# Optimization experiments

Hardware: AMD Instinct MI355X
Metric: run time of the kernel (lower is better)

## Reference

```python
import jax, jax.numpy as jnp
import numpy as np

S, B, E, H = 2048, 4, 1024, 16
HD = E // H
EPS = 1e-8


def _bit_linear(x, W, b):
    """BitNetLinear (eval): ternary weight quant + abs-mean activation scaling."""
    w_scale = jnp.maximum(jnp.mean(jnp.abs(W)), EPS)
    wn = W / w_scale
    qw = jnp.sign(wn) * (jnp.abs(wn) > 0.5).astype(x.dtype)  # {-1,0,1}
    a_scale = jnp.maximum(jnp.mean(jnp.abs(x)), EPS)
    out = (x / a_scale) @ (qw * w_scale).T + b
    return out * a_scale


def setup_inputs() -> dict:
    key = jax.random.key(0)
    ks = jax.random.split(key, 9)
    # xavier-uniform-ish init for [E,E] weights
    lim = float(np.sqrt(6.0 / (E + E)))
    def w(k):
        return jax.random.uniform(k, (E, E), jnp.float32, -lim, lim)
    return {
        "query": jax.random.normal(ks[0], (S, B, E), jnp.float32),
        "Wq": w(ks[1]), "bq": jnp.zeros((E,), jnp.float32),
        "Wk": w(ks[2]), "bk": jnp.zeros((E,), jnp.float32),
        "Wv": w(ks[3]), "bv": jnp.zeros((E,), jnp.float32),
        "Wo": w(ks[4]), "bo": jnp.zeros((E,), jnp.float32),
    }


def reference(query, Wq, bq, Wk, bk, Wv, bv, Wo, bo):
    q = _bit_linear(query, Wq, bq)  # [S,B,E]
    k = _bit_linear(query, Wk, bk)
    v = _bit_linear(query, Wv, bv)
    # [S,B,E] -> [B*H, S, HD]
    def split_heads(t):
        return t.reshape(S, B * H, HD).transpose(1, 0, 2)
    q, k, v = split_heads(q), split_heads(k), split_heads(v)
    scaling = HD ** -0.5
    scores = jnp.einsum("nqd,nkd->nqk", q, k) * scaling  # [B*H,S,S]
    probs = jax.nn.softmax(scores, axis=-1)
    attn = jnp.einsum("nqk,nkd->nqd", probs, v)  # [B*H,S,HD]
    attn = attn.transpose(1, 0, 2).reshape(S, B, E)
    out = _bit_linear(attn, Wo, bo)  # [S,B,E]
    # need_weights=True, average_attn_weights=True -> mean over heads
    attn_weights = probs.reshape(B, H, S, S).mean(axis=1)  # [B,S,S]
    return out, attn_weights
```

## Files before the change

### kernel.cpp

```cpp
#include <hip/hip_runtime.h>


typedef __bf16 bf16_t;
typedef __bf16 bf16x8 __attribute__((ext_vector_type(8)));
typedef float  f32x4  __attribute__((ext_vector_type(4)));

#define MFMA16(Af, Bf, Cv) __builtin_amdgcn_mfma_f32_16x16x32_bf16((Af), (Bf), (Cv), 0, 0, 0)
#define EXP2(x) __builtin_amdgcn_exp2f(x)

constexpr float LOG2E   = 1.4426950408889634f;
constexpr float SHIFT2  = 14.426950408889634f;
constexpr float QSCALE  = 0.125f * LOG2E;

__device__ __forceinline__ void gload16(const void* g, void* l) {
  __builtin_amdgcn_global_load_lds(
      (const __attribute__((address_space(1))) void*)g,
      (__attribute__((address_space(3))) void*)l, 16, 0, 0);
}

__device__ __forceinline__ void stage8k(const bf16_t* __restrict__ g0, int gstride,
                                        char* ldsb, int tid, int w) {
  const int rr = tid >> 3;
  const int cs = ((tid & 7) * 8) ^ ((rr & 7) * 8);
  gload16(g0 + (size_t)rr * gstride + cs, ldsb + w * 1024);
  gload16(g0 + (size_t)(rr + 32) * gstride + cs, ldsb + 4096 + w * 1024);
}

__device__ __forceinline__ void stage8k512(const bf16_t* __restrict__ g0, int gstride,
                                           char* ldsb, int tid) {
  const int rr = tid >> 3;
  const int cs = ((tid & 7) * 8) ^ ((rr & 7) * 8);
  gload16(g0 + (size_t)rr * gstride + cs, ldsb + (tid >> 6) * 1024);
}

__device__ __forceinline__ bf16x8 lds_frag(const char* ldsb, int row, int bytecol) {
  return *(const bf16x8*)(ldsb + row * 128 + (bytecol ^ ((row & 7) << 4)));
}

constexpr int S_ = 2048, B_ = 4, E_ = 1024, H_ = 16, HD_ = 64;
constexpr int M_ = S_ * B_;
constexpr int NH_ = B_ * H_;

constexpr size_t OFF_SCALES = 0;
constexpr size_t OFF_PART   = 256;
constexpr size_t OFF_XB     = 8192;
constexpr size_t SZ_X       = (size_t)M_ * E_ * 2;
constexpr size_t OFF_TQKV   = OFF_XB + SZ_X;
constexpr size_t OFF_TO     = OFF_TQKV + (size_t)3072 * 1024 * 2;
constexpr size_t OFF_QH     = OFF_TO + (size_t)1024 * 1024 * 2;
constexpr size_t SZ_HD      = (size_t)NH_ * S_ * HD_ * 2;
constexpr size_t OFF_KH     = OFF_QH + SZ_HD;
constexpr size_t OFF_VT     = OFF_KH + SZ_HD;
constexpr size_t OFF_STL    = OFF_VT + SZ_HD;
constexpr size_t OFF_ATTN   = OFF_STL + (size_t)NH_ * S_ * 4;

__global__ void k_prep_all(const float4* __restrict__ W0, const float4* __restrict__ W1,
                           const float4* __restrict__ W2, const float4* __restrict__ W3,
                           const float4* __restrict__ X, ushort4* __restrict__ Xb,
                           float* __restrict__ part) {
  const int bid = blockIdx.x;
  float s = 0.f;
  if (bid < 1024) {
    const int seg = bid >> 8, blk = bid & 255;
    const float4* src = (seg == 0) ? W0 : (seg == 1) ? W1 : (seg == 2) ? W2 : W3;
    for (int i = blk * 256 + threadIdx.x; i < 262144; i += 65536) {
      float4 x = src[i];
      s += fabsf(x.x) + fabsf(x.y) + fabsf(x.z) + fabsf(x.w);
    }
  } else {
    for (int i = (bid - 1024) * 256 + threadIdx.x; i < 2097152; i += 65536) {
      float4 v = X[i];
      s += fabsf(v.x) + fabsf(v.y) + fabsf(v.z) + fabsf(v.w);
      ushort4 h;
      h.x = __builtin_bit_cast(unsigned short, (__bf16)v.x);
      h.y = __builtin_bit_cast(unsigned short, (__bf16)v.y);
      h.z = __builtin_bit_cast(unsigned short, (__bf16)v.z);
      h.w = __builtin_bit_cast(unsigned short, (__bf16)v.w);
      Xb[i] = h;
    }
  }
  __shared__ float red[256];
  red[threadIdx.x] = s; __syncthreads();
  for (int st = 128; st > 0; st >>= 1) {
    if (threadIdx.x < st) red[threadIdx.x] += red[threadIdx.x + st];
    __syncthreads();
  }
  if (threadIdx.x == 0) part[bid] = red[0];
}

__global__ void k_finalize(const float* __restrict__ part, float* __restrict__ scales,
                           int r0, int r1) {
  __shared__ float red[256];
  int t = threadIdx.x;
  for (int r = r0; r < r1; ++r) {
    red[t] = part[r * 256 + t];
    __syncthreads();
    for (int st = 128; st > 0; st >>= 1) {
      if (t < st) red[t] += red[t + st];
      __syncthreads();
    }
    if (t == 0) {
      float cnt = (r < 4) ? 1048576.0f : 8388608.0f;
      scales[r] = fmaxf(red[0] / cnt, 1e-8f);
    }
    __syncthreads();
  }
}

__device__ __forceinline__ unsigned short tern_u(float w, float wsc) {
  float wn = w / wsc;
  if (!(fabsf(wn) > 0.5f)) return 0;
  return (wn > 0.f) ? (unsigned short)0x3F80 : (unsigned short)0xBF80;
}

__global__ void k_quantize4(const float4* __restrict__ W0, const float4* __restrict__ W1,
                            const float4* __restrict__ W2, const float4* __restrict__ W3,
                            const float* __restrict__ scales,
                            ushort4* __restrict__ T0, ushort4* __restrict__ T1,
                            ushort4* __restrict__ T2, ushort4* __restrict__ T3) {
  const int seg = blockIdx.x >> 10;
  const int i = (blockIdx.x & 1023) * 256 + threadIdx.x;
  const float4* W = (seg == 0) ? W0 : (seg == 1) ? W1 : (seg == 2) ? W2 : W3;
  ushort4* T = (seg == 0) ? T0 : (seg == 1) ? T1 : (seg == 2) ? T2 : T3;
  float wsc = scales[seg];
  float4 w = W[i];
  ushort4 o;
  o.x = tern_u(w.x, wsc); o.y = tern_u(w.y, wsc);
  o.z = tern_u(w.z, wsc); o.w = tern_u(w.w, wsc);
  T[i] = o;
}

__global__ __launch_bounds__(256) void k_gemm_qkv(
    const bf16_t* __restrict__ Xb, const bf16_t* __restrict__ T,
    const float* __restrict__ scales,
    const float* __restrict__ bq, const float* __restrict__ bk, const float* __restrict__ bv,
    bf16_t* __restrict__ Qh, bf16_t* __restrict__ Kh, bf16_t* __restrict__ Vt) {
  __shared__ char lds[32768];
  const int tid = threadIdx.x, w = tid >> 6, lane = tid & 63;
  const int g = lane >> 4, cc = lane & 15;
  const int l = blockIdx.x;
  const int xcd = l & 7, r = l >> 3;
  const int nIdx = r % 24, mloc = r / 24;
  const int bm = (xcd * 8 + mloc) * 128, bn = nIdx * 128;
  const int wm = (w >> 1) * 64, wn = (w & 1) * 64;
  const int subA = wm >> 6, subB = wn >> 6;
  f32x4 acc[4][4] = {};
  for (int kt = 0; kt < 16; ++kt) {
    const int k0 = kt * 64;
    const bf16_t* xa = &Xb[(size_t)bm * 1024 + k0];
    const bf16_t* tb = &T[(size_t)bn * 1024 + k0];
    stage8k(xa, 1024, lds, tid, w);
    stage8k(xa + 64 * 1024, 1024, lds + 8192, tid, w);
    stage8k(tb, 1024, lds + 16384, tid, w);
    stage8k(tb + 64 * 1024, 1024, lds + 24576, tid, w);
    __syncthreads();
    const char* As = lds + subA * 8192;
    const char* Bs = lds + 16384 + subB * 8192;
    #pragma unroll
    for (int ks = 0; ks < 2; ++ks) {
      bf16x8 af[4], bfr[4];
      #pragma unroll
      for (int i = 0; i < 4; ++i)
        af[i] = lds_frag(As, (wm & 63) + i * 16 + cc, ks * 64 + g * 16);
      #pragma unroll
      for (int j = 0; j < 4; ++j)
        bfr[j] = lds_frag(Bs, (wn & 63) + j * 16 + cc, ks * 64 + g * 16);
      __builtin_amdgcn_s_setprio(1);
      #pragma unroll
      for (int i = 0; i < 4; ++i)
        #pragma unroll
        for (int j = 0; j < 4; ++j)
          acc[i][j] = MFMA16(af[i], bfr[j], acc[i][j]);
      __builtin_amdgcn_s_setprio(0);
    }
    __syncthreads();
  }
  const int seg = bn >> 10;
  const float wsc = scales[seg];
  const float asx = scales[4];
  const float* bias = (seg == 0) ? bq : (seg == 1) ? bk : bv;
  #pragma unroll
  for (int i = 0; i < 4; ++i)
    #pragma unroll
    for (int j = 0; j < 4; ++j)
      #pragma unroll
      for (int r2 = 0; r2 < 4; ++r2) {
        int m = bm + wm + i * 16 + g * 4 + r2;
        int n = bn + wn + j * 16 + cc;
        int e = n & 1023;
        float v = acc[i][j][r2] * wsc + bias[e] * asx;
        int s = m >> 2, b = m & 3, h = e >> 6, d = e & 63;
        if (seg == 0) {
          Qh[((b * 16 + h) * 2048 + s) * 64 + d] = (bf16_t)(v * QSCALE);
        } else if (seg == 1) {
          Kh[((b * 16 + h) * 2048 + s) * 64 + d] = (bf16_t)v;
        } else {
          Vt[((b * 16 + h) * 64 + d) * 2048 + s] = (bf16_t)v;
        }
      }
}

__global__ __launch_bounds__(512) void k_flash(
    const bf16_t* __restrict__ Qh, const bf16_t* __restrict__ Kh,
    const bf16_t* __restrict__ Vt,
    bf16_t* __restrict__ attnb, float* __restrict__ stl) {
  __shared__ char lds[81920];
  char* Ps = lds + 49152;
  const int tid = threadIdx.x, w = tid >> 6, lane = tid & 63;
  const int g = lane >> 4, cc = lane & 15;
  const int l = blockIdx.x;
  const int head = (l & 7) * 8 + ((l >> 3) & 7);
  const int q0 = (l >> 6) * 256;
  const int qbaseA = (head * 2048 + q0 + w * 32 + cc) * 64 + g * 8;
  const int qbaseB = qbaseA + 16 * 64;
  const bf16x8 qa0 = *(const bf16x8*)&Qh[qbaseA];
  const bf16x8 qa1 = *(const bf16x8*)&Qh[qbaseA + 32];
  const bf16x8 qb0 = *(const bf16x8*)&Qh[qbaseB];
  const bf16x8 qb1 = *(const bf16x8*)&Qh[qbaseB + 32];
  const bf16_t* Kb = Kh + (size_t)head * 2048 * 64;
  const bf16_t* Vb = Vt + (size_t)head * 64 * 2048;
  const bf16_t one_b = (bf16_t)1.0f;
  const bf16x8 ones = {one_b, one_b, one_b, one_b, one_b, one_b, one_b, one_b};
  const f32x4 minit = {-SHIFT2, -SHIFT2, -SHIFT2, -SHIFT2};
  f32x4 accOA[4] = {}, accOB[4] = {};
  f32x4 accLA = {}, accLB = {};
  stage8k512(Kb, 64, lds, tid);
  stage8k512(Vb, 2048, lds + 24576, tid);
  stage8k512(Kb + 64 * 64, 64, lds + 8192, tid);
  stage8k512(Vb + 64, 2048, lds + 24576 + 8192, tid);
  int cur = 0;
  for (int t = 0; t < 32; ++t) {
    if (t < 31) asm volatile("s_waitcnt vmcnt(2)" ::: "memory");
    else        asm volatile("s_waitcnt vmcnt(0)" ::: "memory");
    __builtin_amdgcn_s_barrier();
    if (t + 2 < 32) {
      int nb = cur + 2; if (nb >= 3) nb -= 3;
      stage8k512(Kb + (t + 2) * 64 * 64, 64, lds + nb * 8192, tid);
      stage8k512(Vb + (t + 2) * 64, 2048, lds + 24576 + nb * 8192, tid);
    }
    const char* KhL = lds + cur * 8192;
    const char* VtL = lds + 24576 + cur * 8192;
    f32x4 sA[4], sB[4];
    #pragma unroll
    for (int nf = 0; nf < 4; ++nf) { sA[nf] = minit; sB[nf] = minit; }
    __builtin_amdgcn_s_setprio(1);
    #pragma unroll
    for (int nf = 0; nf < 4; ++nf) {
      const int row = nf * 16 + cc;
      bf16x8 kh0 = lds_frag(KhL, row, g * 16);
      bf16x8 kh1 = lds_frag(KhL, row, 64 + g * 16);
      sA[nf] = MFMA16(qa0, kh0, sA[nf]);
      sA[nf] = MFMA16(qa1, kh1, sA[nf]);
      sB[nf] = MFMA16(qb0, kh0, sB[nf]);
      sB[nf] = MFMA16(qb1, kh1, sB[nf]);
    }
    __builtin_amdgcn_s_setprio(0);
    #pragma unroll
    for (int nf = 0; nf < 4; ++nf)
      #pragma unroll
      for (int r = 0; r < 4; ++r) {
        float pA = EXP2(sA[nf][r]);
        float pB = EXP2(sB[nf][r]);
        int rowA = w * 32 + g * 4 + r;
        int rowB = rowA + 16;
        int colb = (nf * 16 + cc) * 2;
        *(bf16_t*)(Ps + ((rowA * 128 + colb) ^ ((rowA & 7) << 4))) = (bf16_t)pA;
        *(bf16_t*)(Ps + ((rowB * 128 + colb) ^ ((rowB & 7) << 4))) = (bf16_t)pB;
      }
    const int prA = w * 32 + cc, prB = prA + 16;
    const int pbA = (prA * 128 + g * 16) ^ ((prA & 7) << 4);
    const int pbB = (prB * 128 + g * 16) ^ ((prB & 7) << 4);
    const bf16x8 paA0 = *(const bf16x8*)(Ps + pbA);
    const bf16x8 paA1 = *(const bf16x8*)(Ps + (pbA ^ 64));
    const bf16x8 paB0 = *(const bf16x8*)(Ps + pbB);
    const bf16x8 paB1 = *(const bf16x8*)(Ps + (pbB ^ 64));
    __builtin_amdgcn_s_setprio(1);
    accLA = MFMA16(paA0, ones, accLA);
    accLA = MFMA16(paA1, ones, accLA);
    accLB = MFMA16(paB0, ones, accLB);
    accLB = MFMA16(paB1, ones, accLB);
    #pragma unroll
    for (int df = 0; df < 4; ++df) {
      const int row = df * 16 + cc;
      bf16x8 v0 = lds_frag(VtL, row, g * 16);
      bf16x8 v1 = lds_frag(VtL, row, 64 + g * 16);
      accOA[df] = MFMA16(paA0, v0, accOA[df]);
      accOA[df] = MFMA16(paA1, v1, accOA[df]);
      accOB[df] = MFMA16(paB0, v0, accOB[df]);
      accOB[df] = MFMA16(paB1, v1, accOB[df]);
    }
    __builtin_amdgcn_s_setprio(0);
    cur = cur + 1; if (cur >= 3) cur = 0;
  }
  const int b = head >> 4, h = head & 15;
  #pragma unroll
  for (int df = 0; df < 4; ++df)
    #pragma unroll
    for (int r = 0; r < 4; ++r) {
      int qA = q0 + w * 32 + g * 4 + r;
      int e = h * 64 + df * 16 + cc;
      attnb[(qA * 4 + b) * 1024 + e] = (bf16_t)(accOA[df][r] / accLA[r]);
      attnb[((qA + 16) * 4 + b) * 1024 + e] = (bf16_t)(accOB[df][r] / accLB[r]);
    }
  if (cc == 0) {
    #pragma unroll
    for (int r = 0; r < 4; ++r) {
      int qA = q0 + w * 32 + g * 4 + r;
      stl[head * 2048 + qA] = accLA[r];
      stl[head * 2048 + qA + 16] = accLB[r];
    }
  }
}

__global__ __launch_bounds__(256) void k_pm(
    const bf16_t* __restrict__ Qh, const bf16_t* __restrict__ Kh,
    const float* __restrict__ stl, float* __restrict__ aw) {
  __shared__ char kbuf[2 * 16384];
  __shared__ float sc_[2048];
  const int tid = threadIdx.x, w = tid >> 6, lane = tid & 63;
  const int g = lane >> 4, cc = lane & 15;
  const int l = blockIdx.x;
  const int q0 = (l & 15) * 128, b = (l >> 4) & 3, z = l >> 6;
  const int kbeg = z * 128;
  for (int i = tid; i < 2048; i += 256) {
    int h = i >> 7, q = i & 127;
    sc_[i] = -log2f(stl[(b * 16 + h) * 2048 + q0 + q]) - SHIFT2;
  }
  __syncthreads();
  stage8k(Kh + ((size_t)(b * 16 + 0) * 2048 + kbeg) * 64, 64, kbuf, tid, w);
  stage8k(Kh + ((size_t)(b * 16 + 1) * 2048 + kbeg) * 64, 64, kbuf + 8192, tid, w);
  int cur = 0;
  float pmA[4][4], pmB[4][4];
  for (int it = 0; it < 16; ++it) {
    const int kt = it >> 3, hp = it & 7;
    const int ktl = kbeg + kt * 64;
    asm volatile("s_waitcnt vmcnt(0)" ::: "memory");
    __builtin_amdgcn_s_barrier();
    if (it + 1 < 16) {
      const int nx = it + 1;
      const int ktn = kbeg + (nx >> 3) * 64, hpn = nx & 7;
      char* nb = kbuf + (cur ^ 1) * 16384;
      stage8k(Kh + ((size_t)(b * 16 + 2 * hpn) * 2048 + ktn) * 64, 64, nb, tid, w);
      stage8k(Kh + ((size_t)(b * 16 + 2 * hpn + 1) * 2048 + ktn) * 64, 64, nb + 8192, tid, w);
    }
    if (hp == 0) {
      #pragma unroll
      for (int nf = 0; nf < 4; ++nf)
        #pragma unroll
        for (int r = 0; r < 4; ++r) { pmA[nf][r] = 0.f; pmB[nf][r] = 0.f; }
    }
    #pragma unroll
    for (int hi = 0; hi < 2; ++hi) {
      const int h = 2 * hp + hi;
      const int head = b * 16 + h;
      const int qbaseA = (head * 2048 + q0 + w * 32 + cc) * 64 + g * 8;
      const int qbaseB = qbaseA + 16 * 64;
      bf16x8 qa0 = *(const bf16x8*)&Qh[qbaseA];
      bf16x8 qa1 = *(const bf16x8*)&Qh[qbaseA + 32];
      bf16x8 qb0 = *(const bf16x8*)&Qh[qbaseB];
      bf16x8 qb1 = *(const bf16x8*)&Qh[qbaseB + 32];
      f32x4 ciA, ciB;
      #pragma unroll
      for (int r = 0; r < 4; ++r) {
        int qloc = w * 32 + g * 4 + r;
        ciA[r] = sc_[h * 128 + qloc];
        ciB[r] = sc_[h * 128 + qloc + 16];
      }
      const char* KhL = kbuf + cur * 16384 + hi * 8192;
      f32x4 sA[4], sB[4];
      #pragma unroll
      for (int nf = 0; nf < 4; ++nf) { sA[nf] = ciA; sB[nf] = ciB; }
      __builtin_amdgcn_s_setprio(1);
      #pragma unroll
      for (int nf = 0; nf < 4; ++nf) {
        const int row = nf * 16 + cc;
        bf16x8 kh0 = lds_frag(KhL, row, g * 16);
        bf16x8 kh1 = lds_frag(KhL, row, 64 + g * 16);
        sA[nf] = MFMA16(qa0, kh0, sA[nf]);
        sA[nf] = MFMA16(qa1, kh1, sA[nf]);
        sB[nf] = MFMA16(qb0, kh0, sB[nf]);
        sB[nf] = MFMA16(qb1, kh1, sB[nf]);
      }
      __builtin_amdgcn_s_setprio(0);
      #pragma unroll
      for (int nf = 0; nf < 4; ++nf)
        #pragma unroll
        for (int r = 0; r < 4; ++r) {
          pmA[nf][r] += EXP2(sA[nf][r]);
          pmB[nf][r] += EXP2(sB[nf][r]);
        }
    }
    if (hp == 7) {
      #pragma unroll
      for (int nf = 0; nf < 4; ++nf)
        #pragma unroll
        for (int r = 0; r < 4; ++r) {
          int qA = q0 + w * 32 + g * 4 + r;
          int k = ktl + nf * 16 + cc;
          aw[((long)(b * 2048 + qA)) * 2048 + k] = pmA[nf][r] * 0.0625f;
          aw[((long)(b * 2048 + qA + 16)) * 2048 + k] = pmB[nf][r] * 0.0625f;
        }
    }
    cur ^= 1;
  }
}

__global__ __launch_bounds__(256) void k_gemm_out(
    const bf16_t* __restrict__ A, const bf16_t* __restrict__ T,
    const float* __restrict__ scales, const float* __restrict__ bo,
    float* __restrict__ out) {
  __shared__ char lds[32768];
  const int tid = threadIdx.x, w = tid >> 6, lane = tid & 63;
  const int g = lane >> 4, cc = lane & 15;
  const int l = blockIdx.x;
  const int xcd = l & 7, r = l >> 3;
  const int nIdx = r & 7, mloc = r >> 3;
  const int bm = (xcd * 8 + mloc) * 128, bn = nIdx * 128;
  const int wm = (w >> 1) * 64, wn = (w & 1) * 64;
  const int subA = wm >> 6, subB = wn >> 6;
  f32x4 acc[4][4] = {};
  for (int kt = 0; kt < 16; ++kt) {
    const int k0 = kt * 64;
    const bf16_t* aa = &A[(size_t)bm * 1024 + k0];
    const bf16_t* tb = &T[(size_t)bn * 1024 + k0];
    stage8k(aa, 1024, lds, tid, w);
    stage8k(aa + 64 * 1024, 1024, lds + 8192, tid, w);
    stage8k(tb, 1024, lds + 16384, tid, w);
    stage8k(tb + 64 * 1024, 1024, lds + 24576, tid, w);
    __syncthreads();
    const char* As = lds + subA * 8192;
    const char* Bs = lds + 16384 + subB * 8192;
    #pragma unroll
    for (int ks = 0; ks < 2; ++ks) {
      bf16x8 af[4], bfr[4];
      #pragma unroll
      for (int i = 0; i < 4; ++i)
        af[i] = lds_frag(As, (wm & 63) + i * 16 + cc, ks * 64 + g * 16);
      #pragma unroll
      for (int j = 0; j < 4; ++j)
        bfr[j] = lds_frag(Bs, (wn & 63) + j * 16 + cc, ks * 64 + g * 16);
      __builtin_amdgcn_s_setprio(1);
      #pragma unroll
      for (int i = 0; i < 4; ++i)
        #pragma unroll
        for (int j = 0; j < 4; ++j)
          acc[i][j] = MFMA16(af[i], bfr[j], acc[i][j]);
      __builtin_amdgcn_s_setprio(0);
    }
    __syncthreads();
  }
  const float wsc = scales[3];
  #pragma unroll
  for (int i = 0; i < 4; ++i)
    #pragma unroll
    for (int j = 0; j < 4; ++j)
      #pragma unroll
      for (int r2 = 0; r2 < 4; ++r2) {
        int m = bm + wm + i * 16 + g * 4 + r2;
        int n = bn + wn + j * 16 + cc;
        out[m * 1024 + n] = acc[i][j][r2] * wsc + bo[n];
      }
}

extern "C" void kernel_launch(void* const* d_in, const int* in_sizes, int n_in,
                              void* d_out, int out_size, void* d_ws, size_t ws_size,
                              hipStream_t stream) {
  (void)in_sizes; (void)n_in; (void)out_size; (void)ws_size;
  const float* query = (const float*)d_in[0];
  const float* Wq = (const float*)d_in[1];
  const float* bq = (const float*)d_in[2];
  const float* Wk = (const float*)d_in[3];
  const float* bk = (const float*)d_in[4];
  const float* Wv = (const float*)d_in[5];
  const float* bv = (const float*)d_in[6];
  const float* Wo = (const float*)d_in[7];
  const float* bo = (const float*)d_in[8];

  char* ws = (char*)d_ws;
  float*  scales = (float*)(ws + OFF_SCALES);
  float*  part   = (float*)(ws + OFF_PART);
  bf16_t* Xb     = (bf16_t*)(ws + OFF_XB);
  bf16_t* Tqkv   = (bf16_t*)(ws + OFF_TQKV);
  bf16_t* To     = (bf16_t*)(ws + OFF_TO);
  bf16_t* Qh     = (bf16_t*)(ws + OFF_QH);
  bf16_t* Kh     = (bf16_t*)(ws + OFF_KH);
  bf16_t* Vt     = (bf16_t*)(ws + OFF_VT);
  float*  Stl    = (float*)(ws + OFF_STL);
  bf16_t* Attn   = (bf16_t*)(ws + OFF_ATTN);

  float* out0 = (float*)d_out;
  float* aw   = out0 + (size_t)M_ * E_;

  k_prep_all<<<1280, 256, 0, stream>>>((const float4*)Wq, (const float4*)Wk,
                                       (const float4*)Wv, (const float4*)Wo,
                                       (const float4*)query, (ushort4*)Xb, part);
  k_finalize<<<1, 256, 0, stream>>>(part, scales, 0, 5);
  k_quantize4<<<4096, 256, 0, stream>>>((const float4*)Wq, (const float4*)Wk,
                                        (const float4*)Wv, (const float4*)Wo, scales,
                                        (ushort4*)Tqkv, (ushort4*)(Tqkv + 1048576),
                                        (ushort4*)(Tqkv + 2097152), (ushort4*)To);

  k_gemm_qkv<<<1536, 256, 0, stream>>>(Xb, Tqkv, scales, bq, bk, bv, Qh, Kh, Vt);
  k_flash<<<512, 512, 0, stream>>>(Qh, Kh, Vt, Attn, Stl);
  k_pm<<<1024, 256, 0, stream>>>(Qh, Kh, Stl, aw);
  k_gemm_out<<<512, 256, 0, stream>>>(Attn, To, scales, bo, out0);
}
```

Before: 296.5 us.

## Fold scale finalize into consumers and merge prob-mean and output GEMM launches

Removes the single-block k_finalize launch: each consumer block (quantize, QKV GEMM epilogue, output GEMM epilogue) now reduces the 256 partial sums itself to get its scale. k_pm and k_gemm_out become one k_tail launch, with blocks split by index between the two jobs so they can run concurrently. This cuts two launches and a serialising one-block kernel. In exchange every block does extra small reductions and barriers, and the merged kernel uses a larger LDS allocation, which may lower occupancy for the GEMM part.

```diff
diff --git a/kernel.cpp b/kernel.cpp
--- a/kernel.cpp
+++ b/kernel.cpp
@@ -35,6 +35,19 @@
 
 __device__ __forceinline__ bf16x8 lds_frag(const char* ldsb, int row, int bytecol) {
   return *(const bf16x8*)(ldsb + row * 128 + (bytecol ^ ((row & 7) << 4)));
+}
+
+__device__ __forceinline__ float scale_from_part(const float* __restrict__ part,
+                                                 int r, float cnt, float* red, int tid) {
+  red[tid] = part[r * 256 + tid];
+  __syncthreads();
+  for (int st = 128; st > 0; st >>= 1) {
+    if (tid < st) red[tid] += red[tid + st];
+    __syncthreads();
+  }
+  float v = fmaxf(red[0] / cnt, 1e-8f);
+  __syncthreads();
+  return v;
 }
 
 constexpr int S_ = 2048, B_ = 4, E_ = 1024, H_ = 16, HD_ = 64;
@@ -88,25 +101,6 @@
   if (threadIdx.x == 0) part[bid] = red[0];
 }
 
-__global__ void k_finalize(const float* __restrict__ part, float* __restrict__ scales,
-                           int r0, int r1) {
-  __shared__ float red[256];
-  int t = threadIdx.x;
-  for (int r = r0; r < r1; ++r) {
-    red[t] = part[r * 256 + t];
-    __syncthreads();
-    for (int st = 128; st > 0; st >>= 1) {
-      if (t < st) red[t] += red[t + st];
-      __syncthreads();
-    }
-    if (t == 0) {
-      float cnt = (r < 4) ? 1048576.0f : 8388608.0f;
-      scales[r] = fmaxf(red[0] / cnt, 1e-8f);
-    }
-    __syncthreads();
-  }
-}
-
 __device__ __forceinline__ unsigned short tern_u(float w, float wsc) {
   float wn = w / wsc;
   if (!(fabsf(wn) > 0.5f)) return 0;
@@ -115,15 +109,16 @@
 
 __global__ void k_quantize4(const float4* __restrict__ W0, const float4* __restrict__ W1,
                             const float4* __restrict__ W2, const float4* __restrict__ W3,
-                            const float* __restrict__ scales,
+                            const float* __restrict__ part,
                             ushort4* __restrict__ T0, ushort4* __restrict__ T1,
                             ushort4* __restrict__ T2, ushort4* __restrict__ T3) {
+  __shared__ float red[256];
   const int seg = blockIdx.x >> 10;
   const int i = (blockIdx.x & 1023) * 256 + threadIdx.x;
   const float4* W = (seg == 0) ? W0 : (seg == 1) ? W1 : (seg == 2) ? W2 : W3;
   ushort4* T = (seg == 0) ? T0 : (seg == 1) ? T1 : (seg == 2) ? T2 : T3;
-  float wsc = scales[seg];
   float4 w = W[i];
+  float wsc = scale_from_part(part, seg, 1048576.0f, red, threadIdx.x);
   ushort4 o;
   o.x = tern_u(w.x, wsc); o.y = tern_u(w.y, wsc);
   o.z = tern_u(w.z, wsc); o.w = tern_u(w.w, wsc);
@@ -132,7 +127,7 @@
 
 __global__ __launch_bounds__(256) void k_gemm_qkv(
     const bf16_t* __restrict__ Xb, const bf16_t* __restrict__ T,
-    const float* __restrict__ scales,
+    const float* __restrict__ part,
     const float* __restrict__ bq, const float* __restrict__ bk, const float* __restrict__ bv,
     bf16_t* __restrict__ Qh, bf16_t* __restrict__ Kh, bf16_t* __restrict__ Vt) {
   __shared__ char lds[32768];
@@ -175,9 +170,10 @@
     }
     __syncthreads();
   }
+  float* red = (float*)lds;
   const int seg = bn >> 10;
-  const float wsc = scales[seg];
-  const float asx = scales[4];
+  const float wsc = scale_from_part(part, seg, 1048576.0f, red, tid);
+  const float asx = scale_from_part(part, 4, 8388608.0f, red, tid);
   const float* bias = (seg == 0) ? bq : (seg == 1) ? bk : bv;
   #pragma unroll
   for (int i = 0; i < 4; ++i)
@@ -312,154 +308,153 @@
   }
 }
 
-__global__ __launch_bounds__(256) void k_pm(
+__global__ __launch_bounds__(256) void k_tail(
     const bf16_t* __restrict__ Qh, const bf16_t* __restrict__ Kh,
-    const float* __restrict__ stl, float* __restrict__ aw) {
-  __shared__ char kbuf[2 * 16384];
-  __shared__ float sc_[2048];
+    const float* __restrict__ stl, float* __restrict__ aw,
+    const bf16_t* __restrict__ A, const bf16_t* __restrict__ T,
+    const float* __restrict__ part, const float* __restrict__ bo,
+    float* __restrict__ out) {
+  __shared__ char lds[40960];
   const int tid = threadIdx.x, w = tid >> 6, lane = tid & 63;
   const int g = lane >> 4, cc = lane & 15;
-  const int l = blockIdx.x;
-  const int q0 = (l & 15) * 128, b = (l >> 4) & 3, z = l >> 6;
-  const int kbeg = z * 128;
-  for (int i = tid; i < 2048; i += 256) {
-    int h = i >> 7, q = i & 127;
-    sc_[i] = -log2f(stl[(b * 16 + h) * 2048 + q0 + q]) - SHIFT2;
-  }
-  __syncthreads();
-  stage8k(Kh + ((size_t)(b * 16 + 0) * 2048 + kbeg) * 64, 64, kbuf, tid, w);
-  stage8k(Kh + ((size_t)(b * 16 + 1) * 2048 + kbeg) * 64, 64, kbuf + 8192, tid, w);
-  int cur = 0;
-  float pmA[4][4], pmB[4][4];
-  for (int it = 0; it < 16; ++it) {
-    const int kt = it >> 3, hp = it & 7;
-    const int ktl = kbeg + kt * 64;
-    asm volatile("s_waitcnt vmcnt(0)" ::: "memory");
-    __builtin_amdgcn_s_barrier();
-    if (it + 1 < 16) {
-      const int nx = it + 1;
-      const int ktn = kbeg + (nx >> 3) * 64, hpn = nx & 7;
-      char* nb = kbuf + (cur ^ 1) * 16384;
-      stage8k(Kh + ((size_t)(b * 16 + 2 * hpn) * 2048 + ktn) * 64, 64, nb, tid, w);
-      stage8k(Kh + ((size_t)(b * 16 + 2 * hpn + 1) * 2048 + ktn) * 64, 64, nb + 8192, tid, w);
-    }
-    if (hp == 0) {
-      #pragma unroll
-      for (int nf = 0; nf < 4; ++nf)
-        #pragma unroll
-        for (int r = 0; r < 4; ++r) { pmA[nf][r] = 0.f; pmB[nf][r] = 0.f; }
-    }
-    #pragma unroll
-    for (int hi = 0; hi < 2; ++hi) {
-      const int h = 2 * hp + hi;
-      const int head = b * 16 + h;
-      const int qbaseA = (head * 2048 + q0 + w * 32 + cc) * 64 + g * 8;
-      const int qbaseB = qbaseA + 16 * 64;
-      bf16x8 qa0 = *(const bf16x8*)&Qh[qbaseA];
-      bf16x8 qa1 = *(const bf16x8*)&Qh[qbaseA + 32];
-      bf16x8 qb0 = *(const bf16x8*)&Qh[qbaseB];
-      bf16x8 qb1 = *(const bf16x8*)&Qh[qbaseB + 32];
-      f32x4 ciA, ciB;
-      #pragma unroll
-      for (int r = 0; r < 4; ++r) {
-        int qloc = w * 32 + g * 4 + r;
-        ciA[r] = sc_[h * 128 + qloc];
-        ciB[r] = sc_[h * 128 + qloc + 16];
-      }
-      const char* KhL = kbuf + cur * 16384 + hi * 8192;
-      f32x4 sA[4], sB[4];
-      #pragma unroll
-      for (int nf = 0; nf < 4; ++nf) { sA[nf] = ciA; sB[nf] = ciB; }
-      __builtin_amdgcn_s_setprio(1);
-      #pragma unroll
-      for (int nf = 0; nf < 4; ++nf) {
-        const int row = nf * 16 + cc;
-        bf16x8 kh0 = lds_frag(KhL, row, g * 16);
-        bf16x8 kh1 = lds_frag(KhL, row, 64 + g * 16);
-        sA[nf] = MFMA16(qa0, kh0, sA[nf]);
-        sA[nf] = MFMA16(qa1, kh1, sA[nf]);
-        sB[nf] = MFMA16(qb0, kh0, sB[nf]);
-        sB[nf] = MFMA16(qb1, kh1, sB[nf]);
-      }
-      __builtin_amdgcn_s_setprio(0);
-      #pragma unroll
-      for (int nf = 0; nf < 4; ++nf)
+  if (blockIdx.x < 1024) {
+    char* kbuf = lds;
+    float* sc_ = (float*)(lds + 32768);
+    const int l = blockIdx.x;
+    const int q0 = (l & 15) * 128, b = (l >> 4) & 3, z = l >> 6;
+    const int kbeg = z * 128;
+    for (int i = tid; i < 2048; i += 256) {
+      int h = i >> 7, q = i & 127;
+      sc_[i] = -log2f(stl[(b * 16 + h) * 2048 + q0 + q]) - SHIFT2;
+    }
+    __syncthreads();
+    stage8k(Kh + ((size_t)(b * 16 + 0) * 2048 + kbeg) * 64, 64, kbuf, tid, w);
+    stage8k(Kh + ((size_t)(b * 16 + 1) * 2048 + kbeg) * 64, 64, kbuf + 8192, tid, w);
+    int cur = 0;
+    float pmA[4][4], pmB[4][4];
+    for (int it = 0; it < 16; ++it) {
+      const int kt = it >> 3, hp = it & 7;
+      const int ktl = kbeg + kt * 64;
+      asm volatile("s_waitcnt vmcnt(0)" ::: "memory");
+      __builtin_amdgcn_s_barrier();
+      if (it + 1 < 16) {
+        const int nx = it + 1;
+        const int ktn = kbeg + (nx >> 3) * 64, hpn = nx & 7;
+        char* nb = kbuf + (cur ^ 1) * 16384;
+        stage8k(Kh + ((size_t)(b * 16 + 2 * hpn) * 2048 + ktn) * 64, 64, nb, tid, w);
+        stage8k(Kh + ((size_t)(b * 16 + 2 * hpn + 1) * 2048 + ktn) * 64, 64, nb + 8192, tid, w);
+      }
+      if (hp == 0) {
+        #pragma unroll
+        for (int nf = 0; nf < 4; ++nf)
+          #pragma unroll
+          for (int r = 0; r < 4; ++r) { pmA[nf][r] = 0.f; pmB[nf][r] = 0.f; }
+      }
+      #pragma unroll
+      for (int hi = 0; hi < 2; ++hi) {
+        const int h = 2 * hp + hi;
+        const int head = b * 16 + h;
+        const int qbaseA = (head * 2048 + q0 + w * 32 + cc) * 64 + g * 8;
+        const int qbaseB = qbaseA + 16 * 64;
+        bf16x8 qa0 = *(const bf16x8*)&Qh[qbaseA];
+        bf16x8 qa1 = *(const bf16x8*)&Qh[qbaseA + 32];
+        bf16x8 qb0 = *(const bf16x8*)&Qh[qbaseB];
+        bf16x8 qb1 = *(const bf16x8*)&Qh[qbaseB + 32];
+        f32x4 ciA, ciB;
         #pragma unroll
         for (int r = 0; r < 4; ++r) {
-          pmA[nf][r] += EXP2(sA[nf][r]);
-          pmB[nf][r] += EXP2(sB[nf][r]);
+          int qloc = w * 32 + g * 4 + r;
+          ciA[r] = sc_[h * 128 + qloc];
+          ciB[r] = sc_[h * 128 + qloc + 16];
         }
-    }
-    if (hp == 7) {
-      #pragma unroll
-      for (int nf = 0; nf < 4; ++nf)
-        #pragma unroll
-        for (int r = 0; r < 4; ++r) {
-          int qA = q0 + w * 32 + g * 4 + r;
-          int k = ktl + nf * 16 + cc;
-          aw[((long)(b * 2048 + qA)) * 2048 + k] = pmA[nf][r] * 0.0625f;
-          aw[((long)(b * 2048 + qA + 16)) * 2048 + k] = pmB[nf][r] * 0.0625f;
+        const char* KhL = kbuf + cur * 16384 + hi * 8192;
+        f32x4 sA[4], sB[4];
+        #pragma unroll
+        for (int nf = 0; nf < 4; ++nf) { sA[nf] = ciA; sB[nf] = ciB; }
+        __builtin_amdgcn_s_setprio(1);
+        #pragma unroll
+        for (int nf = 0; nf < 4; ++nf) {
+          const int row = nf * 16 + cc;
+          bf16x8 kh0 = lds_frag(KhL, row, g * 16);
+          bf16x8 kh1 = lds_frag(KhL, row, 64 + g * 16);
+          sA[nf] = MFMA16(qa0, kh0, sA[nf]);
+          sA[nf] = MFMA16(qa1, kh1, sA[nf]);
+          sB[nf] = MFMA16(qb0, kh0, sB[nf]);
+          sB[nf] = MFMA16(qb1, kh1, sB[nf]);
         }
-    }
-    cur ^= 1;
-  }
-}
-
-__global__ __launch_bounds__(256) void k_gemm_out(
-    const bf16_t* __restrict__ A, const bf16_t* __restrict__ T,
-    const float* __restrict__ scales, const float* __restrict__ bo,
-    float* __restrict__ out) {
-  __shared__ char lds[32768];
-  const int tid = threadIdx.x, w = tid >> 6, lane = tid & 63;
-  const int g = lane >> 4, cc = lane & 15;
-  const int l = blockIdx.x;
-  const int xcd = l & 7, r = l >> 3;
-  const int nIdx = r & 7, mloc = r >> 3;
-  const int bm = (xcd * 8 + mloc) * 128, bn = nIdx * 128;
-  const int wm = (w >> 1) * 64, wn = (w & 1) * 64;
-  const int subA = wm >> 6, subB = wn >> 6;
-  f32x4 acc[4][4] = {};
-  for (int kt = 0; kt < 16; ++kt) {
-    const int k0 = kt * 64;
-    const bf16_t* aa = &A[(size_t)bm * 1024 + k0];
-    const bf16_t* tb = &T[(size_t)bn * 1024 + k0];
-    stage8k(aa, 1024, lds, tid, w);
-    stage8k(aa + 64 * 1024, 1024, lds + 8192, tid, w);
-    stage8k(tb, 1024, lds + 16384, tid, w);
-    stage8k(tb + 64 * 1024, 1024, lds + 24576, tid, w);
-    __syncthreads();
-    const char* As = lds + subA * 8192;
-    const char* Bs = lds + 16384 + subB * 8192;
-    #pragma unroll
-    for (int ks = 0; ks < 2; ++ks) {
-      bf16x8 af[4], bfr[4];
-      #pragma unroll
-      for (int i = 0; i < 4; ++i)
-        af[i] = lds_frag(As, (wm & 63) + i * 16 + cc, ks * 64 + g * 16);
+        __builtin_amdgcn_s_setprio(0);
+        #pragma unroll
+        for (int nf = 0; nf < 4; ++nf)
+          #pragma unroll
+          for (int r = 0; r < 4; ++r) {
+            pmA[nf][r] += EXP2(sA[nf][r]);
+            pmB[nf][r] += EXP2(sB[nf][r]);
+          }
+      }
+      if (hp == 7) {
+        #pragma unroll
+        for (int nf = 0; nf < 4; ++nf)
+          #pragma unroll
+          for (int r = 0; r < 4; ++r) {
+            int qA = q0 + w * 32 + g * 4 + r;
+            int k = ktl + nf * 16 + cc;
+            aw[((long)(b * 2048 + qA)) * 2048 + k] = pmA[nf][r] * 0.0625f;
+            aw[((long)(b * 2048 + qA + 16)) * 2048 + k] = pmB[nf][r] * 0.0625f;
+          }
+      }
+      cur ^= 1;
+    }
+  } else {
+    const int l = blockIdx.x - 1024;
+    const int xcd = l & 7, r = l >> 3;
+    const int nIdx = r & 7, mloc = r >> 3;
+    const int bm = (xcd * 8 + mloc) * 128, bn = nIdx * 128;
+    const int wm = (w >> 1) * 64, wn = (w & 1) * 64;
+    const int subA = wm >> 6, subB = wn >> 6;
+    f32x4 acc[4][4] = {};
+    for (int kt = 0; kt < 16; ++kt) {
+      const int k0 = kt * 64;
+      const bf16_t* aa = &A[(size_t)bm * 1024 + k0];
+      const bf16_t* tb = &T[(size_t)bn * 1024 + k0];
+      stage8k(aa, 1024, lds, tid, w);
+      stage8k(aa + 64 * 1024, 1024, lds + 8192, tid, w);
+      stage8k(tb, 1024, lds + 16384, tid, w);
+      stage8k(tb + 64 * 1024, 1024, lds + 24576, tid, w);
+      __syncthreads();
+      const char* As = lds + subA * 8192;
+      const char* Bs = lds + 16384 + subB * 8192;
+      #pragma unroll
+      for (int ks = 0; ks < 2; ++ks) {
+        bf16x8 af[4], bfr[4];
+        #pragma unroll
+        for (int i = 0; i < 4; ++i)
+          af[i] = lds_frag(As, (wm & 63) + i * 16 + cc, ks * 64 + g * 16);
+        #pragma unroll
+        for (int j = 0; j < 4; ++j)
+          bfr[j] = lds_frag(Bs, (wn & 63) + j * 16 + cc, ks * 64 + g * 16);
+        __builtin_amdgcn_s_setprio(1);
+        #pragma unroll
+        for (int i = 0; i < 4; ++i)
+          #pragma unroll
+          for (int j = 0; j < 4; ++j)
+            acc[i][j] = MFMA16(af[i], bfr[j], acc[i][j]);
+        __builtin_amdgcn_s_setprio(0);
+      }
+      __syncthreads();
+    }
+    float* red = (float*)lds;
+    const float wsc = scale_from_part(part, 3, 1048576.0f, red, tid);
+    #pragma unroll
+    for (int i = 0; i < 4; ++i)
       #pragma unroll
       for (int j = 0; j < 4; ++j)
-        bfr[j] = lds_frag(Bs, (wn & 63) + j * 16 + cc, ks * 64 + g * 16);
-      __builtin_amdgcn_s_setprio(1);
-      #pragma unroll
-      for (int i = 0; i < 4; ++i)
-        #pragma unroll
-        for (int j = 0; j < 4; ++j)
-          acc[i][j] = MFMA16(af[i], bfr[j], acc[i][j]);
-      __builtin_amdgcn_s_setprio(0);
-    }
-    __syncthreads();
-  }
-  const float wsc = scales[3];
-  #pragma unroll
-  for (int i = 0; i < 4; ++i)
-    #pragma unroll
-    for (int j = 0; j < 4; ++j)
-      #pragma unroll
-      for (int r2 = 0; r2 < 4; ++r2) {
-        int m = bm + wm + i * 16 + g * 4 + r2;
-        int n = bn + wn + j * 16 + cc;
-        out[m * 1024 + n] = acc[i][j][r2] * wsc + bo[n];
-      }
+        #pragma unroll
+        for (int r2 = 0; r2 < 4; ++r2) {
+          int m = bm + wm + i * 16 + g * 4 + r2;
+          int n = bn + wn + j * 16 + cc;
+          out[m * 1024 + n] = acc[i][j][r2] * wsc + bo[n];
+        }
+  }
 }
 
 extern "C" void kernel_launch(void* const* d_in, const int* in_sizes, int n_in,
@@ -477,7 +472,6 @@
   const float* bo = (const float*)d_in[8];
 
   char* ws = (char*)d_ws;
-  float*  scales = (float*)(ws + OFF_SCALES);
   float*  part   = (float*)(ws + OFF_PART);
   bf16_t* Xb     = (bf16_t*)(ws + OFF_XB);
   bf16_t* Tqkv   = (bf16_t*)(ws + OFF_TQKV);
@@ -494,14 +488,11 @@
   k_prep_all<<<1280, 256, 0, stream>>>((const float4*)Wq, (const float4*)Wk,
                                        (const float4*)Wv, (const float4*)Wo,
                                        (const float4*)query, (ushort4*)Xb, part);
-  k_finalize<<<1, 256, 0, stream>>>(part, scales, 0, 5);
   k_quantize4<<<4096, 256, 0, stream>>>((const float4*)Wq, (const float4*)Wk,
-                                        (const float4*)Wv, (const float4*)Wo, scales,
+                                        (const float4*)Wv, (const float4*)Wo, part,
                                         (ushort4*)Tqkv, (ushort4*)(Tqkv + 1048576),
                                         (ushort4*)(Tqkv + 2097152), (ushort4*)To);
-
-  k_gemm_qkv<<<1536, 256, 0, stream>>>(Xb, Tqkv, scales, bq, bk, bv, Qh, Kh, Vt);
+  k_gemm_qkv<<<1536, 256, 0, stream>>>(Xb, Tqkv, part, bq, bk, bv, Qh, Kh, Vt);
   k_flash<<<512, 512, 0, stream>>>(Qh, Kh, Vt, Attn, Stl);
-  k_pm<<<1024, 256, 0, stream>>>(Qh, Kh, Stl, aw);
-  k_gemm_out<<<512, 256, 0, stream>>>(Attn, To, scales, bo, out0);
-}
+  k_tail<<<1536, 256, 0, stream>>>(Qh, Kh, Stl, aw, Attn, To, part, bo, out0);
+}
```

After: 293.8 us. Within noise of the previous version (-0.9%).
